# Optimization experiments

Measured on AMD Instinct MI355X. Metric: run time of the kernel, lower is better.

Reference implementation:

```python
import jax, jax.numpy as jnp
import numpy as np

B, C, H, W_ = 64, 3, 224, 224
S = 196            # max_segments
MP = 400           # max_pixels_per_segment
D = 768            # embed_dim (vit_base)


def setup_inputs() -> dict:
    key = jax.random.key(0)
    k1, k2, k3 = jax.random.split(key, 3)
    img = jax.random.normal(k1, (B, C, H, W_), jnp.float32)
    segments = jax.random.randint(k2, (B, H, W_), 0, S, jnp.int32)
    W = jax.random.normal(k3, (C * MP, D), jnp.float32) * 0.02
    b = jnp.zeros((D,), jnp.float32)
    return {"img": img, "segments": segments, "W": W, "b": b}


def _embed_one(img_chw, seg_hw):
    """Gather up to MP pixels per segment (row-major order, like torch bool-mask
    indexing), zero-pad, and flatten in (C, MP) order. Returns [S, C*MP]."""
    c = img_chw.shape[0]
    P = H * W_
    seg = seg_hw.reshape(-1)                                   # [P]
    order = jnp.argsort(seg, stable=True)                      # pixels sorted by segment, row-major within segment
    sorted_seg = seg[order]
    counts = jax.ops.segment_sum(jnp.ones((P,), jnp.int32), seg, num_segments=S)
    starts = jnp.concatenate([jnp.zeros((1,), jnp.int32),
                              jnp.cumsum(counts)[:-1].astype(jnp.int32)])
    rank = jnp.arange(P, dtype=jnp.int32) - starts[sorted_seg]  # index within segment
    valid = rank < MP                                           # truncate overflow pixels
    safe_rank = jnp.minimum(rank, MP - 1)
    pix = img_chw.reshape(c, P).T[order]                        # [P, C]
    buf = jnp.zeros((S, MP, c), img_chw.dtype)
    # (segment, rank) pairs are unique for valid pixels; overflow adds zeros
    buf = buf.at[sorted_seg, safe_rank].add(pix * valid[:, None].astype(img_chw.dtype))
    # torch flattens (C, MP) row-major -> channel-major feature layout
    return buf.transpose(0, 2, 1).reshape(S, c * MP)


def reference(img, segments, W, b):
    feats = jax.vmap(_embed_one)(img, segments)  # [B, S, C*MP]
    return feats @ W + b                          # [B, S, D]
```

## Files before the change

kernel.cpp:

```cpp
#include <hip/hip_runtime.h>
#include <hip/hip_bf16.h>
#include <stdint.h>

#define BATCH 64
#define CHN 3
#define HH 224
#define WW 224
#define PIX (HH * WW)
#define NSEG 196
#define MAXP 400
#define KDIM (CHN * MAXP)
#define DN 768

#define KP4 1216
#define NTK 38
#define MROWS (BATCH * NSEG)

#define CHSZ 512
#define NCH (PIX / CHSZ)

typedef short short8 __attribute__((ext_vector_type(8)));
typedef float f32x4 __attribute__((ext_vector_type(4)));
typedef unsigned int uint4v __attribute__((ext_vector_type(4)));


__device__ __forceinline__ uint32_t packhl(float v) {
    uint32_t x = __float_as_uint(v);
    uint32_t hi = (x + 0x7FFFu + ((x >> 16) & 1u)) >> 16;
    float r = v - __uint_as_float(hi << 16);
    uint32_t y = __float_as_uint(r);
    uint32_t lo = (y + 0x7FFFu + ((y >> 16) & 1u)) >> 16;
    return (hi << 16) | lo;
}

__global__ void k_hist(const int* __restrict__ seg, int* __restrict__ hist) {
    __shared__ int cnt[NSEG];
    int blk = blockIdx.x;
    int b = blk / NCH, ch = blk % NCH;
    int tid = threadIdx.x;
    if (tid < NSEG) cnt[tid] = 0;
    __syncthreads();
    int s = seg[(size_t)b * PIX + ch * CHSZ + tid];
    atomicAdd(&cnt[s], 1);
    __syncthreads();
    if (tid < NSEG) hist[(size_t)blk * NSEG + tid] = cnt[tid];
}

__global__ void k_scan(int* __restrict__ hist, int* __restrict__ counts) {
    int gw = blockIdx.x * 4 + (threadIdx.x >> 6);
    int lane = threadIdx.x & 63;
    int b = gw / NSEG, s = gw - b * NSEG;
    size_t base = (size_t)b * NCH * NSEG + s;
    int v0 = hist[base + (size_t)lane * NSEG];
    int v1 = (lane < NCH - 64) ? hist[base + (size_t)(lane + 64) * NSEG] : 0;
    int p0 = v0, p1 = v1;
    #pragma unroll
    for (int d = 1; d < 64; d <<= 1) {
        int t0 = __shfl_up(p0, d);
        int t1 = __shfl_up(p1, d);
        if (lane >= d) { p0 += t0; p1 += t1; }
    }
    int tot0 = __shfl(p0, 63);
    hist[base + (size_t)lane * NSEG] = p0 - v0;
    if (lane < NCH - 64) hist[base + (size_t)(lane + 64) * NSEG] = tot0 + p1 - v1;
    if (lane == NCH - 64 - 1) counts[gw] = tot0 + p1;
}

__global__ void k_ztail(const int* __restrict__ counts, uint32_t* __restrict__ Apair) {
    int row = blockIdx.x * 4 + (threadIdx.x >> 6);
    int lane = threadIdx.x & 63;
    int cnt = counts[row];
    int start = 3 * min(cnt, MAXP);
    uint32_t* p = Apair + (size_t)row * KP4;
    for (int i = start + lane; i < KP4; i += 64) p[i] = 0u;
}

__global__ void k_scatter(const float* __restrict__ img,
                          const int* __restrict__ seg,
                          const int* __restrict__ offs,
                          uint32_t* __restrict__ Apair) {
    __shared__ int soff[NSEG];
    __shared__ int wcnt[8][NSEG];
    int blk0 = blockIdx.x;
    int wg = (blk0 & 7) * (BATCH * NCH / 8) + (blk0 >> 3);
    int b = wg / NCH, ch = wg % NCH;
    int tid = threadIdx.x;
    int lane = tid & 63, wid = tid >> 6;

    for (int i = tid; i < 8 * NSEG; i += CHSZ) ((int*)wcnt)[i] = 0;
    if (tid < NSEG) soff[tid] = offs[(size_t)wg * NSEG + tid];
    __syncthreads();

    int p = ch * CHSZ + tid;
    int sv = seg[(size_t)b * PIX + p];

    uint64_t m = ~0ull;
    #pragma unroll
    for (int bit = 0; bit < 8; ++bit) {
        uint64_t bal = __ballot((sv >> bit) & 1);
        m &= ((sv >> bit) & 1) ? bal : ~bal;
    }
    int before = __popcll(m & ((1ull << lane) - 1ull));
    int first  = __builtin_ctzll(m);
    if (lane == first) wcnt[wid][sv] = __popcll(m);
    __syncthreads();

    int base = soff[sv];
    for (int w2 = 0; w2 < wid; ++w2) base += wcnt[w2][sv];
    int r = base + before;

    if (r < MAXP) {
        const float* ib = img + (size_t)b * CHN * PIX + p;
        uint32_t* dst = Apair + (size_t)(b * NSEG + sv) * KP4 + 3 * r;
        uint32_t v0 = packhl(ib[0]);
        uint32_t v1 = packhl(ib[PIX]);
        uint32_t v2 = packhl(ib[2 * PIX]);
        dst[0] = v0; dst[1] = v1; dst[2] = v2;
    }
}

__global__ void k_wprep(const float* __restrict__ W, uint32_t* __restrict__ Wt) {
    __shared__ float t[32][33];
    int kt = blockIdx.x, nt = blockIdx.y;
    int tid = threadIdx.x;
    int tx = tid & 31, ty = tid >> 5;
    #pragma unroll
    for (int i = 0; i < 4; ++i) {
        int k = kt * 32 + i * 8 + ty;
        int n = nt * 32 + tx;
        t[i * 8 + ty][tx] = (k < KDIM) ? W[(size_t)k * DN + n] : 0.0f;
    }
    __syncthreads();
    #pragma unroll
    for (int i = 0; i < 4; ++i) {
        int n = nt * 32 + i * 8 + ty;
        int k = kt * 32 + tx;
        int kap = (k < KDIM) ? 3 * (k % MAXP) + (k / MAXP) : k;
        Wt[(size_t)n * KP4 + kap] = packhl(t[tx][i * 8 + ty]);
    }
}

__device__ __forceinline__ void gld16(const void* g, void* l) {
    __builtin_amdgcn_global_load_lds(
        (const __attribute__((address_space(1))) unsigned int*)g,
        (__attribute__((address_space(3))) unsigned int*)l, 16, 0, 0);
}

#define NWG 588
__global__ __launch_bounds__(512, 4) void k_gemm(const uint32_t* __restrict__ A,
                                                 const uint32_t* __restrict__ Bw,
                                                 const float* __restrict__ bias,
                                                 float* __restrict__ Co) {
    __shared__ uint32_t lds[2][2][128 * 32];
    int j = blockIdx.x;
    int xcd = j & 7, sl = j >> 3;
    const int q = NWG / 8, rm = NWG % 8;
    int wgid = (xcd < rm ? xcd * (q + 1) : rm * (q + 1) + (xcd - rm) * q) + sl;
    int bm = wgid / 6, bn = wgid % 6;

    int tid = threadIdx.x;
    int lane = tid & 63, w = tid >> 6;
    int wm = w >> 2, wn = w & 3;
    int r15 = lane & 15, kb = lane >> 4;

    int srow = w * 8 + (lane >> 3);
    int sslot = lane & 7;
    int ssw = sslot ^ (srow & 7);
    size_t aoff0 = (size_t)srow * KP4 + ssw * 4;
    size_t aoff1 = (size_t)(srow + 64) * KP4 + ssw * 4;

    const uint32_t* Ab = A + (size_t)(bm * 128) * KP4;
    const uint32_t* Bb = Bw + (size_t)(bn * 128) * KP4;

    f32x4 acc[4][2] = {};

#define STAGE(buf, kt) do {                                        \
    gld16(Ab + aoff0 + (size_t)(kt) * 32, &lds[buf][0][w * 256]);  \
    gld16(Ab + aoff1 + (size_t)(kt) * 32, &lds[buf][0][2048 + w * 256]); \
    gld16(Bb + aoff0 + (size_t)(kt) * 32, &lds[buf][1][w * 256]);  \
    gld16(Bb + aoff1 + (size_t)(kt) * 32, &lds[buf][1][2048 + w * 256]); \
} while (0)

    STAGE(0, 0);
    __syncthreads();

    int cur = 0;
    for (int kt = 0; kt < NTK; ++kt) {
        if (kt + 1 < NTK) STAGE(cur ^ 1, kt + 1);

        #pragma unroll
        for (int sg = 0; sg < 2; ++sg) {
            union { uint4v u; short8 s; } af[4];
            #pragma unroll
            for (int mi = 0; mi < 4; ++mi) {
                int row = wm * 64 + mi * 16 + r15;
                int slot = (sg * 4 + kb) ^ (row & 7);
                af[mi].u = *(const uint4v*)&lds[cur][0][row * 32 + slot * 4];
            }
            #pragma unroll
            for (int ni = 0; ni < 2; ++ni) {
                int row = wn * 32 + ni * 16 + r15;
                int slot = (sg * 4 + kb) ^ (row & 7);
                union { uint4v u; short8 s; } bf, bs;
                bf.u = *(const uint4v*)&lds[cur][1][row * 32 + slot * 4];
                bs.u.x = (bf.u.x >> 16) | (bf.u.x << 16);
                bs.u.y = (bf.u.y >> 16) | (bf.u.y << 16);
                bs.u.z = (bf.u.z >> 16) | (bf.u.z << 16);
                bs.u.w = (bf.u.w >> 16) | (bf.u.w << 16);
                #pragma unroll
                for (int mi = 0; mi < 4; ++mi) {
                    acc[mi][ni] = __builtin_amdgcn_mfma_f32_16x16x32_bf16(
                        af[mi].s, bf.s, acc[mi][ni], 0, 0, 0);
                    acc[mi][ni] = __builtin_amdgcn_mfma_f32_16x16x32_bf16(
                        af[mi].s, bs.s, acc[mi][ni], 0, 0, 0);
                }
            }
        }

        __syncthreads();
        cur ^= 1;
    }
#undef STAGE

    #pragma unroll
    for (int ni = 0; ni < 2; ++ni) {
        int col = bn * 128 + wn * 32 + ni * 16 + r15;
        float bv = bias[col];
        #pragma unroll
        for (int mi = 0; mi < 4; ++mi) {
            int rbase = bm * 128 + wm * 64 + mi * 16 + kb * 4;
            #pragma unroll
            for (int e = 0; e < 4; ++e)
                Co[(size_t)(rbase + e) * DN + col] = acc[mi][ni][e] + bv;
        }
    }
}

extern "C" void kernel_launch(void* const* d_in, const int* in_sizes, int n_in,
                              void* d_out, int out_size, void* d_ws, size_t ws_size,
                              hipStream_t stream) {
    const float* img = (const float*)d_in[0];
    const int*   seg = (const int*)d_in[1];
    const float* W   = (const float*)d_in[2];
    const float* bia = (const float*)d_in[3];
    float* out = (float*)d_out;

    const size_t APAIR_BYTES = (size_t)MROWS * KP4 * 4;
    const size_t HIST_BYTES  = (size_t)BATCH * NCH * NSEG * 4;
    uint32_t* Apair  = (uint32_t*)d_ws;
    int*      hist   = (int*)((char*)d_ws + APAIR_BYTES);
    int*      counts = (int*)((char*)d_ws + APAIR_BYTES + HIST_BYTES);
    uint32_t* Wt     = (uint32_t*)hist;

    k_hist<<<BATCH * NCH, CHSZ, 0, stream>>>(seg, hist);
    k_scan<<<MROWS / 4, 256, 0, stream>>>(hist, counts);
    k_ztail<<<MROWS / 4, 256, 0, stream>>>(counts, Apair);
    k_scatter<<<BATCH * NCH, CHSZ, 0, stream>>>(img, seg, hist, Apair);
    k_wprep<<<dim3(NTK, DN / 32), 256, 0, stream>>>(W, Wt);

    k_gemm<<<NWG, 512, 0, stream>>>(Apair, Wt, bia, out);
}
```

Baseline: 247.5 us.

## Relax GEMM barriers with vmcnt waits, merge tail-zeroing into weight prep

```diff
diff --git a/kernel.cpp b/kernel.cpp
--- a/kernel.cpp
+++ b/kernel.cpp
@@ -47,32 +47,17 @@
 }
 
 __global__ void k_scan(int* __restrict__ hist, int* __restrict__ counts) {
-    int gw = blockIdx.x * 4 + (threadIdx.x >> 6);
-    int lane = threadIdx.x & 63;
-    int b = gw / NSEG, s = gw - b * NSEG;
-    size_t base = (size_t)b * NCH * NSEG + s;
-    int v0 = hist[base + (size_t)lane * NSEG];
-    int v1 = (lane < NCH - 64) ? hist[base + (size_t)(lane + 64) * NSEG] : 0;
-    int p0 = v0, p1 = v1;
-    #pragma unroll
-    for (int d = 1; d < 64; d <<= 1) {
-        int t0 = __shfl_up(p0, d);
-        int t1 = __shfl_up(p1, d);
-        if (lane >= d) { p0 += t0; p1 += t1; }
-    }
-    int tot0 = __shfl(p0, 63);
-    hist[base + (size_t)lane * NSEG] = p0 - v0;
-    if (lane < NCH - 64) hist[base + (size_t)(lane + 64) * NSEG] = tot0 + p1 - v1;
-    if (lane == NCH - 64 - 1) counts[gw] = tot0 + p1;
-}
-
-__global__ void k_ztail(const int* __restrict__ counts, uint32_t* __restrict__ Apair) {
-    int row = blockIdx.x * 4 + (threadIdx.x >> 6);
-    int lane = threadIdx.x & 63;
-    int cnt = counts[row];
-    int start = 3 * min(cnt, MAXP);
-    uint32_t* p = Apair + (size_t)row * KP4;
-    for (int i = start + lane; i < KP4; i += 64) p[i] = 0u;
+    int i = blockIdx.x * blockDim.x + threadIdx.x;
+    if (i >= BATCH * NSEG) return;
+    int b = i / NSEG, s = i % NSEG;
+    int run = 0;
+    for (int c = 0; c < NCH; ++c) {
+        size_t idx = ((size_t)b * NCH + c) * NSEG + s;
+        int t = hist[idx];
+        hist[idx] = run;
+        run += t;
+    }
+    counts[i] = run;
 }
 
 __global__ void k_scatter(const float* __restrict__ img,
@@ -119,10 +104,22 @@
     }
 }
 
-__global__ void k_wprep(const float* __restrict__ W, uint32_t* __restrict__ Wt) {
+#define WPREP_BLKS (NTK * (DN / 32))
+__global__ void k_prep(const float* __restrict__ W, uint32_t* __restrict__ Wt,
+                       const int* __restrict__ counts, uint32_t* __restrict__ Apair) {
+    int blk = blockIdx.x;
+    int tid = threadIdx.x;
+    if (blk >= WPREP_BLKS) {
+        int row = (blk - WPREP_BLKS) * 4 + (tid >> 6);
+        int lane = tid & 63;
+        int cnt = counts[row];
+        int start = 3 * min(cnt, MAXP);
+        uint32_t* p = Apair + (size_t)row * KP4;
+        for (int i = start + lane; i < KP4; i += 64) p[i] = 0u;
+        return;
+    }
     __shared__ float t[32][33];
-    int kt = blockIdx.x, nt = blockIdx.y;
-    int tid = threadIdx.x;
+    int kt = blk % NTK, nt = blk / NTK;
     int tx = tid & 31, ty = tid >> 5;
     #pragma unroll
     for (int i = 0; i < 4; ++i) {
@@ -182,11 +179,16 @@
 } while (0)
 
     STAGE(0, 0);
-    __syncthreads();
 
     int cur = 0;
     for (int kt = 0; kt < NTK; ++kt) {
-        if (kt + 1 < NTK) STAGE(cur ^ 1, kt + 1);
+        if (kt + 1 < NTK) {
+            STAGE(cur ^ 1, kt + 1);
+            asm volatile("s_waitcnt vmcnt(4)" ::: "memory");
+        } else {
+            asm volatile("s_waitcnt vmcnt(0)" ::: "memory");
+        }
+        __builtin_amdgcn_s_barrier();
 
         #pragma unroll
         for (int sg = 0; sg < 2; ++sg) {
@@ -217,7 +219,7 @@
             }
         }
 
-        __syncthreads();
+        __builtin_amdgcn_s_barrier();
         cur ^= 1;
     }
 #undef STAGE
@@ -253,10 +255,9 @@
     uint32_t* Wt     = (uint32_t*)hist;
 
     k_hist<<<BATCH * NCH, CHSZ, 0, stream>>>(seg, hist);
-    k_scan<<<MROWS / 4, 256, 0, stream>>>(hist, counts);
-    k_ztail<<<MROWS / 4, 256, 0, stream>>>(counts, Apair);
+    k_scan<<<(BATCH * NSEG + 255) / 256, 256, 0, stream>>>(hist, counts);
     k_scatter<<<BATCH * NCH, CHSZ, 0, stream>>>(img, seg, hist, Apair);
-    k_wprep<<<dim3(NTK, DN / 32), 256, 0, stream>>>(W, Wt);
+    k_prep<<<WPREP_BLKS + MROWS / 4, 256, 0, stream>>>(W, Wt, counts, Apair);
 
     k_gemm<<<NWG, 512, 0, stream>>>(Apair, Wt, bia, out);
 }
```

Measured after the change: 232.8 us. 1.06x faster.
